# Optimization experiments

Hardware: AMD Instinct MI355X
Metric: run time of the kernel (lower is better)

Reference implementation:

```python
import jax, jax.numpy as jnp
from jax import lax
import numpy as np

K = 10            # size_feat
N_MU = 10         # number of mean-PSF components
NCH = K * K + N_MU  # 110 depthwise channels
KLEN = 65         # precomputed kernel length


def setup_inputs() -> dict:
    key = jax.random.key(0)
    ks = jax.random.split(key, 12)
    B, C, H, W = 1, 3, 256, 256
    img = jax.random.uniform(ks[0], (B, C, H, W), jnp.float32)
    zernike = jax.random.normal(ks[1], (B, H, W, 35), jnp.float32)
    # pos displacements (first 2 channels) scaled to a few pixels
    zernike = zernike.at[..., :2].multiply(2.0)
    fc1_w = jax.random.normal(ks[2], (200, 33), jnp.float32) / np.float32(np.sqrt(33))
    fc1_b = jax.random.normal(ks[3], (200,), jnp.float32) * 0.01
    fc2_w = jax.random.normal(ks[4], (200, 200), jnp.float32) / np.float32(np.sqrt(200))
    fc2_b = jax.random.normal(ks[5], (200,), jnp.float32) * 0.01
    fc3_w = jax.random.normal(ks[6], (100, 200), jnp.float32) * 0.01
    fc3_b = jnp.zeros((100,), jnp.float32)
    basis_left = jax.random.normal(ks[7], (KLEN, K), jnp.float32) * 0.05
    basis_right = jax.random.normal(ks[8], (KLEN, K), jnp.float32) * 0.05
    mu = jax.random.uniform(ks[9], (KLEN, N_MU), jnp.float32) / np.float32(KLEN)
    return dict(img=img, zernike=zernike, fc1_w=fc1_w, fc1_b=fc1_b,
                fc2_w=fc2_w, fc2_b=fc2_b, fc3_w=fc3_w, fc3_b=fc3_b,
                basis_left=basis_left, basis_right=basis_right, mu=mu, ksize=65)


def _grid_sample_border(img, pos):
    """Bilinear grid_sample, padding_mode='border', align_corners=False.
    img: (B,C,H,W), pos: (B,H,W,2) pixel displacements (x,y)."""
    B, C, H, W = img.shape
    yy, xx = jnp.meshgrid(jnp.arange(H, dtype=jnp.float32),
                          jnp.arange(W, dtype=jnp.float32), indexing='ij')
    grid = jnp.stack((xx, yy), -1)                       # (H,W,2)
    wh = jnp.array([W - 1, H - 1], jnp.float32)
    flow = 2.0 * (grid[None] + pos) / wh - 1.0           # (B,H,W,2) in [-1,1]
    ix = ((flow[..., 0] + 1.0) * W - 1.0) * 0.5
    iy = ((flow[..., 1] + 1.0) * H - 1.0) * 0.5
    ix = jnp.clip(ix, 0.0, W - 1)
    iy = jnp.clip(iy, 0.0, H - 1)
    x0 = jnp.floor(ix); y0 = jnp.floor(iy)
    wx = ix - x0;       wy = iy - y0
    x0i = jnp.clip(x0.astype(jnp.int32), 0, W - 1)
    y0i = jnp.clip(y0.astype(jnp.int32), 0, H - 1)
    x1i = jnp.clip(x0i + 1, 0, W - 1)
    y1i = jnp.clip(y0i + 1, 0, H - 1)

    def bilerp(im, x0i, x1i, y0i, y1i, wx, wy):
        g = lambda yi, xi: im[:, yi, xi]                 # (C,H,W)
        top = g(y0i, x0i) * (1 - wx) + g(y0i, x1i) * wx
        bot = g(y1i, x0i) * (1 - wx) + g(y1i, x1i) * wx
        return top * (1 - wy) + bot * wy

    return jax.vmap(bilerp)(img, x0i, x1i, y0i, y1i, wx, wy)


def _depthwise(x, w, pad_axis, pad):
    # x: (N, NCH, H, W); w: (NCH,1,kh,kw). Reflect 'same' padding on pad_axis.
    cfg = [(0, 0)] * 4
    cfg[pad_axis] = (pad, pad)
    xp = jnp.pad(x, cfg, mode='reflect')
    return lax.conv_general_dilated(
        xp, w, (1, 1), 'VALID',
        dimension_numbers=('NCHW', 'OIHW', 'NCHW'),
        feature_group_count=x.shape[1])


def _forward(img, zernike, fc1_w, fc1_b, fc2_w, fc2_b, fc3_w, fc3_b,
             basis_left, basis_right, mu, ksize):
    B, C, H, W = img.shape
    pad = ksize // 2
    # --- grid-sample warp ---
    tilt = _grid_sample_border(img, zernike[..., :2])    # (B,C,H,W)
    # --- per-pixel MLP -> PSF coefficients ---
    f = zernike[..., 2:]                                  # (B,H,W,33)
    h = jax.nn.leaky_relu(f @ fc1_w.T + fc1_b)
    h = jax.nn.leaky_relu(h @ fc2_w.T + fc2_b)
    coef = h @ fc3_w.T + fc3_b                            # (B,H,W,100)
    weight = jnp.concatenate(
        [coef, jnp.ones((B, H, W, N_MU), coef.dtype)], -1)  # (B,H,W,110)
    # --- elementwise weight multiply ---
    big = jnp.concatenate([tilt, jnp.ones_like(tilt)], 1)  # (B,2C,H,W)
    big = big[..., None] * weight[:, None]                 # (B,2C,H,W,110)
    x = big.reshape(B * 2 * C, H, W, NCH).transpose(0, 3, 1, 2)  # (B*2C,110,H,W)
    # --- separable depthwise blur kernels (outer products Z_i x X_j + mu) ---
    wl = jnp.concatenate([jnp.repeat(basis_left.T, K, axis=0), mu.T], 0)  # (110,klen)
    wr = jnp.concatenate([jnp.tile(basis_right.T, (K, 1)), mu.T], 0)      # (110,klen)
    wl = wl[:, None, :, None]                              # (110,1,klen,1)
    wr = wr[:, None, None, :]                              # (110,1,1,klen)
    y = _depthwise(x, wl, 2, pad)
    y = _depthwise(y, wr, 3, pad)
    d = y.reshape(B, 2 * C, NCH, H, W)
    out = jnp.sum(d[:, :3], axis=2) / jnp.sum(d[:, 3:], axis=2)  # (B,3,H,W)
    return out


def reference(img, zernike, fc1_w, fc1_b, fc2_w, fc2_b, fc3_w, fc3_b,
              basis_left, basis_right, mu, ksize):
    return _forward(img, zernike, fc1_w, fc1_b, fc2_w, fc2_b, fc3_w, fc3_b,
                    basis_left, basis_right, mu, ksize)
```

## Files before the change

kernel.cpp:

```cpp
#include <hip/hip_runtime.h>

#define HW 65536

typedef __attribute__((ext_vector_type(8))) short short8;
typedef __attribute__((ext_vector_type(4))) float float4v;

__device__ __forceinline__ int refl(int i){ if (i < 0) i = -i; if (i > 255) i = 510 - i; return i; }
__device__ __forceinline__ float lrelu(float x){ return x > 0.f ? x : 0.01f * x; }
__device__ __forceinline__ unsigned int f2bf(float x){
  union { float f; unsigned int u; } v; v.f = x;
  unsigned int r = v.u + 0x7fff + ((v.u >> 16) & 1);
  return r >> 16;
}

#define W2OFF 13312
#define W3OFF 59904
__global__ __launch_bounds__(256) void k_gsprep(const float* __restrict__ img,
    const float* __restrict__ zern,
    const float* __restrict__ w1, const float* __restrict__ w2,
    const float* __restrict__ w3, const float* __restrict__ bl,
    const float* __restrict__ br, const float* __restrict__ mu,
    float* __restrict__ tilt, unsigned short* __restrict__ wbf,
    unsigned short* __restrict__ Tt, float* __restrict__ mucp){
  __shared__ float sm[650];
  __shared__ float sq[10];
  int bid = blockIdx.x;
  int tid = threadIdx.x;
  if (bid < 256){
    int x = tid, y = bid;
    int pix = y * 256 + x;
    float px = zern[pix * 35 + 0], py = zern[pix * 35 + 1];
    float ix = ((float)x + px) * (256.f / 255.f) - 0.5f;
    float iy = ((float)y + py) * (256.f / 255.f) - 0.5f;
    ix = fminf(fmaxf(ix, 0.f), 255.f);
    iy = fminf(fmaxf(iy, 0.f), 255.f);
    float x0f = floorf(ix), y0f = floorf(iy);
    float wx = ix - x0f, wy = iy - y0f;
    int x0 = (int)x0f, y0 = (int)y0f;
    int x1 = min(x0 + 1, 255), y1 = min(y0 + 1, 255);
    #pragma unroll
    for (int c = 0; c < 3; ++c){
      const float* im = img + c * HW;
      float g00 = im[y0 * 256 + x0], g01 = im[y0 * 256 + x1];
      float g10 = im[y1 * 256 + x0], g11 = im[y1 * 256 + x1];
      float top = g00 * (1.f - wx) + g01 * wx;
      float bot = g10 * (1.f - wx) + g11 * wx;
      tilt[c * HW + pix] = top * (1.f - wy) + bot * wy;
    }
  } else if (bid < 768){
    int i = (bid - 256) * 256 + tid;
    if (i < 84992){
      if (i < 208 * 64){
        int n = i >> 6, k = i & 63;
        float v = (n < 200 && k < 33) ? w1[n * 33 + k] : 0.f;
        wbf[i] = (unsigned short)f2bf(v);
      } else if (i < W2OFF + 208 * 224){
        int j = i - W2OFF; int n = j / 224, k = j - n * 224;
        float v = (n < 200 && k < 200) ? w2[n * 200 + k] : 0.f;
        wbf[i] = (unsigned short)f2bf(v);
      } else {
        int j = i - W3OFF; int n = j / 224, k = j - n * 224;
        float v = (n < 100 && k < 200) ? w3[n * 200 + k] : 0.f;
        wbf[i] = (unsigned short)f2bf(v);
      }
    } else {
      int e = i - 84992;
      int t = e / 1536, rem = e - t * 1536;
      int m = rem / 96, k = rem - m * 96;
      int d = k - m;
      float v = 0.f;
      if (d >= 0 && d <= 64){
        if (t < 10)      v = bl[d * 10 + t];
        else if (t < 20) v = mu[d * 10 + (t - 10)];
        else             v = br[d * 10 + (t - 20)];
      }
      Tt[e] = (unsigned short)f2bf(v);
    }
  } else {
    for (int e = tid; e < 650; e += 256) sm[e] = mu[e];
    __syncthreads();
    if (tid < 10){
      float s = 0.f;
      for (int u = 0; u < 65; ++u) s += sm[u * 10 + tid];
      sq[tid] = s * s;
    }
    __syncthreads();
    if (tid == 0){
      float m = 0.f;
      #pragma unroll
      for (int mm = 0; mm < 10; ++mm) m += sq[mm];
      mucp[0] = m;
    }
  }
}

#define HSTR 232
__global__ __launch_bounds__(256) void k_mlp(const float* __restrict__ zern,
    const float* __restrict__ b1f, const float* __restrict__ b2f,
    const float* __restrict__ b3f, const unsigned short* __restrict__ wbf,
    float* __restrict__ coefp){
  __shared__ char smem[29696];
  unsigned short* H1 = (unsigned short*)smem;
  float*          H3 = (float*)smem;
  unsigned short* XB = (unsigned short*)(smem + 14848);
  unsigned short* H2 = XB;
  int tid = threadIdx.x;
  int pix0 = blockIdx.x * 32;
  int lane = tid & 63, wv = tid >> 6;
  int ln = lane & 15, qd = lane >> 4;

  for (int e = tid; e < 1152; e += 256) ((int*)XB)[e] = 0;
  for (int e = tid; e < 384; e += 256){
    int m = e / 12, j = e - m * 12;
    ((int*)H1)[m * 116 + 104 + j] = 0;
  }
  __syncthreads();
  for (int e = tid; e < 32 * 33; e += 256){
    int m = e / 33, k = e - m * 33;
    XB[m * 72 + k] = (unsigned short)f2bf(zern[(pix0 + m) * 35 + 2 + k]);
  }
  __syncthreads();

  for (int nt = wv; nt < 13; nt += 4){
    int n = nt * 16 + ln;
    short8 b0 = *(const short8*)(wbf + n * 64 + qd * 8);
    short8 b1 = *(const short8*)(wbf + n * 64 + 32 + qd * 8);
    float bv = (n < 200) ? b1f[n] : 0.f;
    #pragma unroll
    for (int mt = 0; mt < 2; ++mt){
      float4v acc = {bv, bv, bv, bv};
      short8 a0 = *(const short8*)(XB + (mt * 16 + ln) * 72 + qd * 8);
      short8 a1 = *(const short8*)(XB + (mt * 16 + ln) * 72 + 32 + qd * 8);
      acc = __builtin_amdgcn_mfma_f32_16x16x32_bf16(a0, b0, acc, 0, 0, 0);
      acc = __builtin_amdgcn_mfma_f32_16x16x32_bf16(a1, b1, acc, 0, 0, 0);
      #pragma unroll
      for (int r = 0; r < 4; ++r)
        H1[(mt * 16 + qd * 4 + r) * HSTR + n] = (unsigned short)f2bf(lrelu(acc[r]));
    }
  }
  __syncthreads();

  for (int e = tid; e < 384; e += 256){
    int m = e / 12, j = e - m * 12;
    ((int*)H2)[m * 116 + 104 + j] = 0;
  }
  {
    const unsigned short* w2p = wbf + W2OFF;
    for (int nt = wv; nt < 13; nt += 4){
      int n = nt * 16 + ln;
      short8 bf[7];
      #pragma unroll
      for (int kc = 0; kc < 7; ++kc)
        bf[kc] = *(const short8*)(w2p + n * 224 + kc * 32 + qd * 8);
      float bv = (n < 200) ? b2f[n] : 0.f;
      #pragma unroll
      for (int mt = 0; mt < 2; ++mt){
        float4v acc = {bv, bv, bv, bv};
        #pragma unroll
        for (int kc = 0; kc < 7; ++kc){
          short8 af = *(const short8*)(H1 + (mt * 16 + ln) * HSTR + kc * 32 + qd * 8);
          acc = __builtin_amdgcn_mfma_f32_16x16x32_bf16(af, bf[kc], acc, 0, 0, 0);
        }
        #pragma unroll
        for (int r = 0; r < 4; ++r)
          H2[(mt * 16 + qd * 4 + r) * HSTR + n] = (unsigned short)f2bf(lrelu(acc[r]));
      }
    }
  }
  __syncthreads();

  {
    const unsigned short* w3p = wbf + W3OFF;
    for (int nt = wv; nt < 7; nt += 4){
      int n = nt * 16 + ln;
      short8 bf[7];
      #pragma unroll
      for (int kc = 0; kc < 7; ++kc)
        bf[kc] = *(const short8*)(w3p + n * 224 + kc * 32 + qd * 8);
      float bv = (n < 100) ? b3f[n] : 0.f;
      #pragma unroll
      for (int mt = 0; mt < 2; ++mt){
        float4v acc = {bv, bv, bv, bv};
        #pragma unroll
        for (int kc = 0; kc < 7; ++kc){
          short8 af = *(const short8*)(H2 + (mt * 16 + ln) * HSTR + kc * 32 + qd * 8);
          acc = __builtin_amdgcn_mfma_f32_16x16x32_bf16(af, bf[kc], acc, 0, 0, 0);
        }
        #pragma unroll
        for (int r = 0; r < 4; ++r)
          H3[(mt * 16 + qd * 4 + r) * 113 + n] = acc[r];
      }
    }
  }
  __syncthreads();

  for (int e = tid; e < 3200; e += 256){
    int n = e >> 5, m = e & 31;
    coefp[n * HW + pix0 + m] = H3[m * 113 + n];
  }
}

#define VB 344
__global__ __launch_bounds__(256) void k_vconv14(const float* __restrict__ tilt,
    const float* __restrict__ coefp, const unsigned short* __restrict__ Tt,
    unsigned short* __restrict__ sbuf, unsigned short* __restrict__ smu){
  __shared__ __align__(16) unsigned short sxb[2][16 * VB];
  int tid = threadIdx.x;
  int bid = blockIdx.x;
  int lane = tid & 63, wv = tid >> 6;
  int ln = lane & 15, qd = lane >> 4;
  int col = tid & 15, seg = tid >> 4;
  int r0 = seg * 20;

  int goff[20];
  #pragma unroll
  for (int q = 0; q < 20; ++q) goff[q] = refl(r0 + q - 32) * 256 + col;

  for (int e = tid; e < 768; e += 256){
    int b = e / 384, r = e - b * 384;
    int cc = r / 24, rp = r - cc * 24;
    sxb[b][cc * VB + 320 + rp] = 0;
  }

  if (bid < 640){
    int s = bid & 15;
    int cj = bid >> 4;
    int c = cj / 10, j = cj - c * 10;
    int x0 = s * 16;
    float treg[20];
    if (c < 3){
      const float* tc = tilt + c * HW + x0;
      #pragma unroll
      for (int q = 0; q < 20; ++q) treg[q] = tc[goff[q]];
    }
    float pf[20];
    {
      const float* cq = coefp + j * HW + x0;
      #pragma unroll
      for (int q = 0; q < 20; ++q) pf[q] = cq[goff[q]];
    }
    float4v acc[4];
    #pragma unroll
    for (int t = 0; t < 4; ++t) acc[t] = (float4v){0.f, 0.f, 0.f, 0.f};
    for (int i = 0; i < 10; ++i){
      int us = i & 1;
      unsigned short* sb = sxb[us];
      #pragma unroll
      for (int q = 0; q < 10; ++q){
        float v0 = pf[2 * q], v1 = pf[2 * q + 1];
        if (c < 3){ v0 *= treg[2 * q]; v1 *= treg[2 * q + 1]; }
        *(unsigned int*)&sb[col * VB + r0 + 2 * q] = f2bf(v0) | (f2bf(v1) << 16);
      }
      __syncthreads();
      if (i < 9){
        const float* cn = coefp + ((i + 1) * 10 + j) * HW + x0;
        #pragma unroll
        for (int q = 0; q < 20; ++q) pf[q] = cn[goff[q]];
      }
      const unsigned short* ta = Tt + i * 1536 + ln * 96 + qd * 8;
      short8 A0 = *(const short8*)(ta);
      short8 A1 = *(const short8*)(ta + 32);
      short8 A2 = *(const short8*)(ta + 64);
      #pragma unroll
      for (int t = 0; t < 4; ++t){
        int yt = wv * 4 + t;
        const unsigned short* bp = sb + ln * VB + yt * 16 + qd * 8;
        short8 B0 = *(const short8*)(bp);
        short8 B1 = *(const short8*)(bp + 32);
        short8 B2 = *(const short8*)(bp + 64);
        acc[t] = __builtin_amdgcn_mfma_f32_16x16x32_bf16(A0, B0, acc[t], 0, 0, 0);
        acc[t] = __builtin_amdgcn_mfma_f32_16x16x32_bf16(A1, B1, acc[t], 0, 0, 0);
        acc[t] = __builtin_amdgcn_mfma_f32_16x16x32_bf16(A2, B2, acc[t], 0, 0, 0);
      }
    }
    unsigned short* S = sbuf + (c * 10 + j) * HW + x0 + ln;
    #pragma unroll
    for (int t = 0; t < 4; ++t){
      int yt = wv * 4 + t;
      #pragma unroll
      for (int r = 0; r < 4; ++r)
        S[(yt * 16 + qd * 4 + r) * 256] = (unsigned short)f2bf(acc[t][r]);
    }
  } else {
    int b2 = bid - 640;
    int c = b2 >> 4, s = b2 & 15;
    int x0 = s * 16;
    const float* tc = tilt + c * HW + x0;
    float tv[20];
    #pragma unroll
    for (int q = 0; q < 20; ++q) tv[q] = tc[goff[q]];
    #pragma unroll
    for (int q = 0; q < 10; ++q){
      *(unsigned int*)&sxb[0][col * VB + r0 + 2 * q] = f2bf(tv[2 * q]) | (f2bf(tv[2 * q + 1]) << 16);
    }
    __syncthreads();
    for (int m = 0; m < 10; ++m){
      const unsigned short* ta = Tt + (10 + m) * 1536 + ln * 96 + qd * 8;
      short8 A0 = *(const short8*)(ta);
      short8 A1 = *(const short8*)(ta + 32);
      short8 A2 = *(const short8*)(ta + 64);
      float4v acc[4];
      #pragma unroll
      for (int t = 0; t < 4; ++t) acc[t] = (float4v){0.f, 0.f, 0.f, 0.f};
      #pragma unroll
      for (int t = 0; t < 4; ++t){
        int yt = wv * 4 + t;
        const unsigned short* bp = sxb[0] + ln * VB + yt * 16 + qd * 8;
        short8 B0 = *(const short8*)(bp);
        short8 B1 = *(const short8*)(bp + 32);
        short8 B2 = *(const short8*)(bp + 64);
        acc[t] = __builtin_amdgcn_mfma_f32_16x16x32_bf16(A0, B0, acc[t], 0, 0, 0);
        acc[t] = __builtin_amdgcn_mfma_f32_16x16x32_bf16(A1, B1, acc[t], 0, 0, 0);
        acc[t] = __builtin_amdgcn_mfma_f32_16x16x32_bf16(A2, B2, acc[t], 0, 0, 0);
      }
      unsigned short* S = smu + (c * 10 + m) * HW + x0 + ln;
      #pragma unroll
      for (int t = 0; t < 4; ++t){
        int yt = wv * 4 + t;
        #pragma unroll
        for (int r = 0; r < 4; ++r)
          S[(yt * 16 + qd * 4 + r) * 256] = (unsigned short)f2bf(acc[t][r]);
      }
    }
  }
}

#define HS2 344
__global__ __launch_bounds__(256) void k_hconv9(const unsigned short* __restrict__ sbuf,
    const unsigned short* __restrict__ smu, const unsigned short* __restrict__ Tt,
    float* __restrict__ part){
  __shared__ __align__(16) unsigned short sxb[16 * HS2];
  int tid = threadIdx.x;
  int grp = blockIdx.x >> 4;
  int yt  = blockIdx.x & 15;
  int y0 = yt * 16;
  int lane = tid & 63, wv = tid >> 6;
  int ln = lane & 15, qd = lane >> 4;
  int srow = tid >> 4, scol = tid & 15;
  int isbr = (grp < 8);
  int tgt, h;
  if (isbr){ tgt = grp >> 1; h = grp & 1; }
  else     { int g2 = grp - 8; tgt = g2 >> 1; h = g2 & 1; }
  const unsigned short* base = isbr ? (sbuf + tgt * 10 * HW) : (smu + tgt * 10 * HW);
  int tbase = isbr ? 20 : 10;

  for (int e = tid; e < 384; e += 256){
    int rr = e / 24, cp = e - rr * 24;
    sxb[rr * HS2 + 320 + cp] = 0;
  }

  int gx[20];
  #pragma unroll
  for (int q = 0; q < 20; ++q) gx[q] = refl(scol * 20 - 32 + q);

  float4v acc[4];
  #pragma unroll
  for (int t = 0; t < 4; ++t) acc[t] = (float4v){0.f, 0.f, 0.f, 0.f};

  for (int p = 0; p < 5; ++p){
    int col = h * 5 + p;
    const unsigned short* plane = base + col * HW + (y0 + srow) * 256;
    __syncthreads();
    unsigned short v[20];
    #pragma unroll
    for (int q = 0; q < 20; ++q) v[q] = plane[gx[q]];
    #pragma unroll
    for (int q = 0; q < 10; ++q){
      *(unsigned int*)&sxb[srow * HS2 + scol * 20 + 2 * q] =
          (unsigned int)v[2 * q] | ((unsigned int)v[2 * q + 1] << 16);
    }
    __syncthreads();
    const unsigned short* ta = Tt + (tbase + col) * 1536 + ln * 96 + qd * 8;
    short8 A0 = *(const short8*)(ta);
    short8 A1 = *(const short8*)(ta + 32);
    short8 A2 = *(const short8*)(ta + 64);
    #pragma unroll
    for (int t = 0; t < 4; ++t){
      int wt = wv * 4 + t;
      const unsigned short* bp = sxb + ln * HS2 + wt * 16 + qd * 8;
      short8 B0 = *(const short8*)(bp);
      short8 B1 = *(const short8*)(bp + 32);
      short8 B2 = *(const short8*)(bp + 64);
      acc[t] = __builtin_amdgcn_mfma_f32_16x16x32_bf16(A0, B0, acc[t], 0, 0, 0);
      acc[t] = __builtin_amdgcn_mfma_f32_16x16x32_bf16(A1, B1, acc[t], 0, 0, 0);
      acc[t] = __builtin_amdgcn_mfma_f32_16x16x32_bf16(A2, B2, acc[t], 0, 0, 0);
    }
  }
  #pragma unroll
  for (int t = 0; t < 4; ++t){
    int wt = wv * 4 + t;
    float4 res = {acc[t][0], acc[t][1], acc[t][2], acc[t][3]};
    *(float4*)(part + grp * HW + (y0 + ln) * 256 + wt * 16 + qd * 4) = res;
  }
}

__global__ __launch_bounds__(256) void k_final(const float* __restrict__ part,
                                               const float* __restrict__ mucp,
                                               float* __restrict__ out){
  int pix = blockIdx.x * 256 + threadIdx.x;
  float muC = mucp[0];
  float den = part[6 * HW + pix] + part[7 * HW + pix] + muC;
  float inv = 1.f / den;
  #pragma unroll
  for (int c = 0; c < 3; ++c){
    float num = part[(2 * c) * HW + pix] + part[(2 * c + 1) * HW + pix]
              + part[(8 + 2 * c) * HW + pix] + part[(9 + 2 * c) * HW + pix];
    out[c * HW + pix] = num * inv;
  }
}

extern "C" void kernel_launch(void* const* d_in, const int* in_sizes, int n_in,
                              void* d_out, int out_size, void* d_ws, size_t ws_size,
                              hipStream_t stream) {
  const float* img  = (const float*)d_in[0];
  const float* zern = (const float*)d_in[1];
  const float* w1   = (const float*)d_in[2];
  const float* b1   = (const float*)d_in[3];
  const float* w2   = (const float*)d_in[4];
  const float* b2   = (const float*)d_in[5];
  const float* w3   = (const float*)d_in[6];
  const float* b3   = (const float*)d_in[7];
  const float* bl   = (const float*)d_in[8];
  const float* br   = (const float*)d_in[9];
  const float* mu   = (const float*)d_in[10];
  float* out = (float*)d_out;

  float* w     = (float*)d_ws;
  float* tilt  = w;
  float* coefp = w + 3 * HW;
  float* part  = w + 3 * HW;
  unsigned short* sbuf = (unsigned short*)(w + 103 * HW);
  unsigned short* smu  = (unsigned short*)(w + 143 * HW);
  unsigned short* wbf  = (unsigned short*)(w + 103 * HW);
  unsigned short* Tt   = (unsigned short*)(w + 173 * HW);
  float* mucp = (float*)(Tt + 46080);

  k_gsprep<<<769, 256, 0, stream>>>(img, zern, w1, w2, w3, bl, br, mu, tilt, wbf, Tt, mucp);
  k_mlp<<<2048, 256, 0, stream>>>(zern, b1, b2, b3, wbf, coefp);
  k_vconv14<<<688, 256, 0, stream>>>(tilt, coefp, Tt, sbuf, smu);
  k_hconv9<<<224, 256, 0, stream>>>(sbuf, smu, Tt, part);
  k_final<<<256, 256, 0, stream>>>(part, mucp, out);
}
```

Measured before the change: 156.8 us.

## Store MLP coefficients as fp16 and fuse grid-sample into MLP kernel

The MLP kernel now writes its 100 per-pixel coefficients as packed fp16 instead of fp32. This halves the intermediate buffer traffic between the MLP and the vertical convolution, which now reads 16-bit values and converts them. The bilinear grid-sample computing the tilted image moves out of the prep kernel into the MLP kernel, shrinking the prep launch. Workspace offsets are compacted to match the smaller buffer. The cost is fp16 rounding of the coefficients before the bf16 conversion, which slightly reduces precision.

```diff
diff --git a/kernel.cpp b/kernel.cpp
--- a/kernel.cpp
+++ b/kernel.cpp
@@ -12,43 +12,26 @@
   unsigned int r = v.u + 0x7fff + ((v.u >> 16) & 1);
   return r >> 16;
 }
+__device__ __forceinline__ unsigned short f2h(float x){
+  union { _Float16 h; unsigned short u; } v; v.h = (_Float16)x; return v.u;
+}
+__device__ __forceinline__ float h2f(unsigned short u){
+  union { _Float16 h; unsigned short u; } v; v.u = u; return (float)v.h;
+}
 
 #define W2OFF 13312
 #define W3OFF 59904
-__global__ __launch_bounds__(256) void k_gsprep(const float* __restrict__ img,
-    const float* __restrict__ zern,
-    const float* __restrict__ w1, const float* __restrict__ w2,
-    const float* __restrict__ w3, const float* __restrict__ bl,
-    const float* __restrict__ br, const float* __restrict__ mu,
-    float* __restrict__ tilt, unsigned short* __restrict__ wbf,
+__global__ __launch_bounds__(256) void k_prep(const float* __restrict__ w1,
+    const float* __restrict__ w2, const float* __restrict__ w3,
+    const float* __restrict__ bl, const float* __restrict__ br,
+    const float* __restrict__ mu, unsigned short* __restrict__ wbf,
     unsigned short* __restrict__ Tt, float* __restrict__ mucp){
   __shared__ float sm[650];
   __shared__ float sq[10];
   int bid = blockIdx.x;
   int tid = threadIdx.x;
-  if (bid < 256){
-    int x = tid, y = bid;
-    int pix = y * 256 + x;
-    float px = zern[pix * 35 + 0], py = zern[pix * 35 + 1];
-    float ix = ((float)x + px) * (256.f / 255.f) - 0.5f;
-    float iy = ((float)y + py) * (256.f / 255.f) - 0.5f;
-    ix = fminf(fmaxf(ix, 0.f), 255.f);
-    iy = fminf(fmaxf(iy, 0.f), 255.f);
-    float x0f = floorf(ix), y0f = floorf(iy);
-    float wx = ix - x0f, wy = iy - y0f;
-    int x0 = (int)x0f, y0 = (int)y0f;
-    int x1 = min(x0 + 1, 255), y1 = min(y0 + 1, 255);
-    #pragma unroll
-    for (int c = 0; c < 3; ++c){
-      const float* im = img + c * HW;
-      float g00 = im[y0 * 256 + x0], g01 = im[y0 * 256 + x1];
-      float g10 = im[y1 * 256 + x0], g11 = im[y1 * 256 + x1];
-      float top = g00 * (1.f - wx) + g01 * wx;
-      float bot = g10 * (1.f - wx) + g11 * wx;
-      tilt[c * HW + pix] = top * (1.f - wy) + bot * wy;
-    }
-  } else if (bid < 768){
-    int i = (bid - 256) * 256 + tid;
+  if (bid < 512){
+    int i = bid * 256 + tid;
     if (i < 84992){
       if (i < 208 * 64){
         int n = i >> 6, k = i & 63;
@@ -95,13 +78,14 @@
 }
 
 #define HSTR 232
-__global__ __launch_bounds__(256) void k_mlp(const float* __restrict__ zern,
+__global__ __launch_bounds__(256) void k_mlp(const float* __restrict__ img,
+    const float* __restrict__ zern,
     const float* __restrict__ b1f, const float* __restrict__ b2f,
     const float* __restrict__ b3f, const unsigned short* __restrict__ wbf,
-    float* __restrict__ coefp){
+    float* __restrict__ tilt, unsigned short* __restrict__ coefb){
   __shared__ char smem[29696];
-  unsigned short* H1 = (unsigned short*)smem;
-  float*          H3 = (float*)smem;
+  unsigned short* H1  = (unsigned short*)smem;
+  unsigned short* H3u = (unsigned short*)smem;
   unsigned short* XB = (unsigned short*)(smem + 14848);
   unsigned short* H2 = XB;
   int tid = threadIdx.x;
@@ -109,6 +93,27 @@
   int lane = tid & 63, wv = tid >> 6;
   int ln = lane & 15, qd = lane >> 4;
 
+  if (tid < 96){
+    int m = tid & 31, c = tid >> 5;
+    int pix = pix0 + m;
+    int x = pix & 255, y = pix >> 8;
+    float px = zern[pix * 35 + 0], py = zern[pix * 35 + 1];
+    float ix = ((float)x + px) * (256.f / 255.f) - 0.5f;
+    float iy = ((float)y + py) * (256.f / 255.f) - 0.5f;
+    ix = fminf(fmaxf(ix, 0.f), 255.f);
+    iy = fminf(fmaxf(iy, 0.f), 255.f);
+    float x0f = floorf(ix), y0f = floorf(iy);
+    float wx = ix - x0f, wy = iy - y0f;
+    int x0 = (int)x0f, y0 = (int)y0f;
+    int x1 = min(x0 + 1, 255), y1 = min(y0 + 1, 255);
+    const float* im = img + c * HW;
+    float g00 = im[y0 * 256 + x0], g01 = im[y0 * 256 + x1];
+    float g10 = im[y1 * 256 + x0], g11 = im[y1 * 256 + x1];
+    float top = g00 * (1.f - wx) + g01 * wx;
+    float bot = g10 * (1.f - wx) + g11 * wx;
+    tilt[c * HW + pix] = top * (1.f - wy) + bot * wy;
+  }
+
   for (int e = tid; e < 1152; e += 256) ((int*)XB)[e] = 0;
   for (int e = tid; e < 384; e += 256){
     int m = e / 12, j = e - m * 12;
@@ -188,21 +193,23 @@
         }
         #pragma unroll
         for (int r = 0; r < 4; ++r)
-          H3[(mt * 16 + qd * 4 + r) * 113 + n] = acc[r];
+          H3u[(mt * 16 + qd * 4 + r) * 113 + n] = f2h(acc[r]);
       }
     }
   }
   __syncthreads();
 
-  for (int e = tid; e < 3200; e += 256){
-    int n = e >> 5, m = e & 31;
-    coefp[n * HW + pix0 + m] = H3[m * 113 + n];
+  for (int e = tid; e < 1600; e += 256){
+    int n = e >> 4, mp = e & 15;
+    unsigned int lo = H3u[(2 * mp) * 113 + n];
+    unsigned int hi = H3u[(2 * mp + 1) * 113 + n];
+    *(unsigned int*)(coefb + n * HW + pix0 + 2 * mp) = lo | (hi << 16);
   }
 }
 
 #define VB 344
-__global__ __launch_bounds__(256) void k_vconv14(const float* __restrict__ tilt,
-    const float* __restrict__ coefp, const unsigned short* __restrict__ Tt,
+__global__ __launch_bounds__(256) void k_vconv15(const float* __restrict__ tilt,
+    const unsigned short* __restrict__ coefb, const unsigned short* __restrict__ Tt,
     unsigned short* __restrict__ sbuf, unsigned short* __restrict__ smu){
   __shared__ __align__(16) unsigned short sxb[2][16 * VB];
   int tid = threadIdx.x;
@@ -233,9 +240,9 @@
       #pragma unroll
       for (int q = 0; q < 20; ++q) treg[q] = tc[goff[q]];
     }
-    float pf[20];
+    unsigned short pf[20];
     {
-      const float* cq = coefp + j * HW + x0;
+      const unsigned short* cq = coefb + j * HW + x0;
       #pragma unroll
       for (int q = 0; q < 20; ++q) pf[q] = cq[goff[q]];
     }
@@ -245,15 +252,24 @@
     for (int i = 0; i < 10; ++i){
       int us = i & 1;
       unsigned short* sb = sxb[us];
-      #pragma unroll
-      for (int q = 0; q < 10; ++q){
-        float v0 = pf[2 * q], v1 = pf[2 * q + 1];
-        if (c < 3){ v0 *= treg[2 * q]; v1 *= treg[2 * q + 1]; }
-        *(unsigned int*)&sb[col * VB + r0 + 2 * q] = f2bf(v0) | (f2bf(v1) << 16);
+      if (c < 3){
+        #pragma unroll
+        for (int q = 0; q < 10; ++q){
+          float v0 = h2f(pf[2 * q]) * treg[2 * q];
+          float v1 = h2f(pf[2 * q + 1]) * treg[2 * q + 1];
+          *(unsigned int*)&sb[col * VB + r0 + 2 * q] = f2bf(v0) | (f2bf(v1) << 16);
+        }
+      } else {
+        #pragma unroll
+        for (int q = 0; q < 10; ++q){
+          float v0 = h2f(pf[2 * q]);
+          float v1 = h2f(pf[2 * q + 1]);
+          *(unsigned int*)&sb[col * VB + r0 + 2 * q] = f2bf(v0) | (f2bf(v1) << 16);
+        }
       }
       __syncthreads();
       if (i < 9){
-        const float* cn = coefp + ((i + 1) * 10 + j) * HW + x0;
+        const unsigned short* cn = coefb + ((i + 1) * 10 + j) * HW + x0;
         #pragma unroll
         for (int q = 0; q < 20; ++q) pf[q] = cn[goff[q]];
       }
@@ -425,19 +441,19 @@
   const float* mu   = (const float*)d_in[10];
   float* out = (float*)d_out;
 
-  float* w     = (float*)d_ws;
-  float* tilt  = w;
-  float* coefp = w + 3 * HW;
-  float* part  = w + 3 * HW;
-  unsigned short* sbuf = (unsigned short*)(w + 103 * HW);
-  unsigned short* smu  = (unsigned short*)(w + 143 * HW);
-  unsigned short* wbf  = (unsigned short*)(w + 103 * HW);
-  unsigned short* Tt   = (unsigned short*)(w + 173 * HW);
+  float* w = (float*)d_ws;
+  float* tilt = w;
+  unsigned short* coefb = (unsigned short*)(w + 3 * HW);
+  float* part = w + 3 * HW;
+  unsigned short* sbuf = (unsigned short*)(w + 53 * HW);
+  unsigned short* smu  = (unsigned short*)(w + 73 * HW);
+  unsigned short* wbf  = (unsigned short*)(w + 53 * HW);
+  unsigned short* Tt   = (unsigned short*)(w + 88 * HW);
   float* mucp = (float*)(Tt + 46080);
 
-  k_gsprep<<<769, 256, 0, stream>>>(img, zern, w1, w2, w3, bl, br, mu, tilt, wbf, Tt, mucp);
-  k_mlp<<<2048, 256, 0, stream>>>(zern, b1, b2, b3, wbf, coefp);
-  k_vconv14<<<688, 256, 0, stream>>>(tilt, coefp, Tt, sbuf, smu);
+  k_prep<<<513, 256, 0, stream>>>(w1, w2, w3, bl, br, mu, wbf, Tt, mucp);
+  k_mlp<<<2048, 256, 0, stream>>>(img, zern, b1, b2, b3, wbf, tilt, coefb);
+  k_vconv15<<<688, 256, 0, stream>>>(tilt, coefb, Tt, sbuf, smu);
   k_hconv9<<<224, 256, 0, stream>>>(sbuf, smu, Tt, part);
   k_final<<<256, 256, 0, stream>>>(part, mucp, out);
 }
```

New measurement: 151.8 us. 3.2% less time.
